# Performance work log

Hardware: AMD Instinct MI355X
Metric: run time of the kernel (lower is better)

Reference implementation:

```python
import jax, jax.numpy as jnp
from jax import lax
import numpy as np


def _pava_pool_idx(y):
    """Pool index per position for the non-decreasing PAVA isotonic fit of 1-D y.
    Stack-based pool-adjacent-violators: sums/cnts hold active pools, top is stack size.
    Returns int pool index (length n) mapping each position to its final pool."""
    n = y.shape[0]

    def step(carry, yi):
        su, ct, top = carry
        su = su.at[top].set(yi)
        ct = ct.at[top].set(1.0)
        top = top + 1

        def cond(s):
            s_, c_, t_ = s
            # violation: mean(pool[t-1]) < mean(pool[t-2]); cross-multiplied (cnts > 0).
            # safe when t_ == 1: index -1 holds zeros -> 0 < 0 is False.
            viol = s_[t_ - 1] * c_[t_ - 2] < s_[t_ - 2] * c_[t_ - 1]
            return (t_ >= 2) & viol

        def body(s):
            s_, c_, t_ = s
            s_ = s_.at[t_ - 2].add(s_[t_ - 1])
            c_ = c_.at[t_ - 2].add(c_[t_ - 1])
            return s_, c_, t_ - 1

        carry = lax.while_loop(cond, body, (su, ct, top))
        return carry, None

    init = (jnp.zeros(n, y.dtype), jnp.zeros(n, y.dtype), jnp.int32(0))
    (su, ct, top), _ = lax.scan(step, init, y)
    # pool j covers positions [ends[j-1], ends[j]); unused pools have ct == 0.
    ends = jnp.cumsum(ct)
    idx = jnp.searchsorted(ends, jnp.arange(n, dtype=ct.dtype), side='right')
    return idx


def _isotonic_nonincreasing_clip0(y):
    """sklearn isotonic_regression(y, y_min=0, increasing=False).
    Pools of the non-increasing fit of y == pools of the non-decreasing fit of -y.
    Final fitted value on each pool is the pool mean of y, clipped at 0."""
    n = y.shape[0]
    idx = _pava_pool_idx(-y)
    sums = jax.ops.segment_sum(y, idx, num_segments=n)
    cnts = jax.ops.segment_sum(jnp.ones_like(y), idx, num_segments=n)
    means = sums / jnp.maximum(cnts, 1.0)
    return jnp.maximum(means[idx], 0.0)


def _prox_owl(beta, weights):
    n = beta.shape[0]
    abs_b = jnp.abs(beta)
    order = jnp.argsort(-abs_b)               # descending |beta|
    iso_in = abs_b[order] - weights
    fit = _isotonic_nonincreasing_clip0(iso_in)
    # inverse permutation: idxs[ix] = arange(n)
    inv = jnp.zeros(n, jnp.int32).at[order].set(jnp.arange(n, dtype=jnp.int32))
    return jnp.sign(beta) * fit[inv]


def reference(u, x, weights):
    diff = (u - x).reshape(-1)
    proxd = _prox_owl(diff, weights)
    return x + proxd.reshape(x.shape)


def setup_inputs() -> dict:
    key = jax.random.key(0)
    k1, k2, k3 = jax.random.split(key, 3)
    shape = (1, 3, 224, 224)
    n = int(np.prod(shape))
    u = jax.random.normal(k1, shape, dtype=jnp.float32)
    x = jax.random.normal(k2, shape, dtype=jnp.float32)
    # OWL weights must be nonincreasing and nonnegative
    w = jnp.sort(jax.random.uniform(k3, (n,), dtype=jnp.float32))[::-1] * 0.01
    return {"u": u, "x": x, "weights": w}
```

## Files before the change

### kernel.cpp

```cpp
#include <hip/hip_runtime.h>
#include <stdint.h>
#include <math.h>

typedef unsigned long long u64;

#define NB 16384
#define BCAP 128
#define NSEG 8192
#define PBLK 64
#define NBLK (NSEG / PBLK)
#define MAXLC 24


__global__ void k_init(const float* __restrict__ u, const float* __restrict__ x,
                       u64* __restrict__ keyPad, int* __restrict__ cursor, int n) {
  int i = blockIdx.x * blockDim.x + threadIdx.x;
  if (i >= n) return;
  float d = u[i] - x[i];
  float ad = fabsf(d);
  u64 key = ((u64)__float_as_uint(ad) << 32) | (unsigned)(~(unsigned)i);
  double v = erf(0.5 * (double)ad);
  int b = (int)(v * (double)NB);
  b = min(max(b, 0), NB - 1);
  int pos = atomicAdd(&cursor[b], 1);
  if (pos < BCAP) keyPad[(size_t)b * BCAP + pos] = key;
}

__global__ void k_scan(const int* __restrict__ cursor, int* __restrict__ descOff) {
  __shared__ int part[1024];
  int t = threadIdx.x;
  const int S = NB / 1024;
  int loc[S];
  int s0 = t * S;
  int sum = 0;
  for (int j = 0; j < S; ++j) { loc[j] = cursor[NB - 1 - (s0 + j)]; sum += loc[j]; }
  part[t] = sum;
  __syncthreads();
  for (int d = 1; d < 1024; d <<= 1) {
    int v = (t >= d) ? part[t - d] : 0;
    __syncthreads();
    part[t] += v;
    __syncthreads();
  }
  int run = part[t] - sum;
  for (int j = 0; j < S; ++j) {
    int b = NB - 1 - (s0 + j);
    descOff[b] = run;
    run += loc[j];
  }
}

__global__ void __launch_bounds__(64) k_bsort(const u64* __restrict__ keyPad,
                                              u64* __restrict__ keyB,
                                              const int* __restrict__ descOff,
                                              const int* __restrict__ cursor) {
  int b = blockIdx.x;
  int cnt = min(cursor[b], BCAP);
  if (cnt == 0) return;
  int start = descOff[b];
  int lane = threadIdx.x;
  const u64* src = keyPad + (size_t)b * BCAP;
  if (cnt == 1) {
    if (lane == 0) keyB[start] = src[0];
    return;
  }
  if (cnt <= 64) {
    int W = 2;
    while (W < cnt) W <<= 1;
    u64 v0 = (lane < cnt) ? src[lane] : 0ull;
    for (int k = 2; k <= W; k <<= 1) {
      for (int j = k >> 1; j >= 1; j >>= 1) {
        bool up = ((lane & j) == 0);
        bool desc = ((lane & k) == 0);
        u64 p = __shfl_xor(v0, j);
        u64 mx = (v0 > p) ? v0 : p, mn = (v0 > p) ? p : v0;
        v0 = (up == desc) ? mx : mn;
      }
    }
    if (lane < cnt) keyB[start + lane] = v0;
  } else {
    u64 v0 = (lane < cnt) ? src[lane] : 0ull;
    u64 v1 = (lane + 64 < cnt) ? src[lane + 64] : 0ull;
    for (int k = 2; k <= 128; k <<= 1) {
      for (int j = k >> 1; j >= 1; j >>= 1) {
        if (j == 64) {
          u64 mx = (v0 > v1) ? v0 : v1;
          u64 mn = (v0 > v1) ? v1 : v0;
          v0 = mx; v1 = mn;
        } else {
          bool up = ((lane & j) == 0);
          bool desc0 = ((lane & k) == 0);
          bool desc1 = (((lane + 64) & k) == 0);
          u64 p0 = __shfl_xor(v0, j);
          u64 p1 = __shfl_xor(v1, j);
          u64 mx0 = (v0 > p0) ? v0 : p0, mn0 = (v0 > p0) ? p0 : v0;
          v0 = (up == desc0) ? mx0 : mn0;
          u64 mx1 = (v1 > p1) ? v1 : p1, mn1 = (v1 > p1) ? p1 : v1;
          v1 = (up == desc1) ? mx1 : mn1;
        }
      }
    }
    if (lane < cnt) keyB[start + lane] = v0;
    if (lane + 64 < cnt) keyB[start + lane + 64] = v1;
  }
}


__device__ __forceinline__ void merge_pair(
    int sL, int sR,
    int* shR, int* stRk, float* shS, float* shC, float* stS, float* stC,
    float* __restrict__ pSum, float* __restrict__ pCnt,
    int* __restrict__ prv, int* __restrict__ nxt) {
  int rR = shR[sR];
  if (rR < 0) return;
  if (shR[sL] < 0) {
    shR[sL] = rR; shS[sL] = shS[sR]; shC[sL] = shC[sR];
    stRk[sL] = stRk[sR]; stS[sL] = stS[sR]; stC[sL] = stC[sR];
    return;
  }
  int lR = stRk[sL];
  float lS = stS[sL], lC = stC[sL];
  float rS = shS[sR], rC = shC[sR];
  nxt[lR] = rR; prv[rR] = lR;
  if (rS * lC > lS * rC) {
    float MS = lS + rS, MC = lC + rC;
    int Mr = lR;
    bool rtail = (rR == stRk[sR]);
    pCnt[rR] = 0.f;
    int nx = nxt[rR];
    nxt[Mr] = nx; if (nx >= 0) prv[nx] = Mr;
    for (;;) {
      int pp = prv[Mr];
      if (pp >= 0) {
        float ps = pSum[pp], pc = pCnt[pp];
        if (MS * pc > ps * MC) {
          MS += ps; MC += pc;
          pCnt[Mr] = 0.f;
          int mn = nxt[Mr];
          nxt[pp] = mn; if (mn >= 0) prv[mn] = pp;
          Mr = pp;
          continue;
        }
      }
      int qq = nxt[Mr];
      if (qq >= 0) {
        float qs = pSum[qq], qc = pCnt[qq];
        if (qs * MC > MS * qc) {
          MS += qs; MC += qc;
          pCnt[qq] = 0.f;
          if (qq == stRk[sR]) rtail = true;
          int qn = nxt[qq];
          nxt[Mr] = qn; if (qn >= 0) prv[qn] = Mr;
          continue;
        }
      }
      break;
    }
    pSum[Mr] = MS; pCnt[Mr] = MC;
    if (Mr == shR[sL]) { shS[sL] = MS; shC[sL] = MC; }
    if (rtail) { stRk[sL] = Mr; stS[sL] = MS; stC[sL] = MC; }
    else       { stRk[sL] = stRk[sR]; stS[sL] = stS[sR]; stC[sL] = stC[sR]; }
  } else {
    stRk[sL] = stRk[sR]; stS[sL] = stS[sR]; stC[sL] = stC[sR];
  }
}

__global__ void __launch_bounds__(64) k_pava_seg(
    const u64* __restrict__ key, const float* __restrict__ w,
    float* __restrict__ pSum, float* __restrict__ pCnt,
    int* __restrict__ prv, int* __restrict__ nxt,
    int* __restrict__ headR2, int* __restrict__ tailR2,
    float* __restrict__ headS2, float* __restrict__ headC2,
    float* __restrict__ tailS2, float* __restrict__ tailC2,
    int n, int Lc, int stride) {
  __shared__ float yv[PBLK * (MAXLC + 1)];
  __shared__ float sS[PBLK * (MAXLC + 1)];
  __shared__ float sC[PBLK * (MAXLC + 1)];
  __shared__ int bHR[PBLK], bTR[PBLK];
  __shared__ float bHS[PBLK], bHC[PBLK], bTS[PBLK], bTC[PBLK];

  int t = threadIdx.x;
  int blk = blockIdx.x;
  int B0 = blk * PBLK * Lc;
  const unsigned* kh = (const unsigned*)key;
  int tot = PBLK * Lc;
  for (int i = t; i < tot; i += PBLK) {
    int g = B0 + i;
    float v = 0.f;
    if (g < n) v = __uint_as_float(kh[2 * g + 1]) - w[g];
    yv[(i / Lc) * stride + (i % Lc)] = v;
  }
  __syncthreads();

  int s = B0 + t * Lc;
  int e = min(s + Lc, n);
  if (s >= e) {
    bHR[t] = -1; bTR[t] = -1;
  } else {
    int cnt = e - s;
    int lb = t * stride;
    float ts = 0.f, tc = 0.f;
    float ss = 0.f, sc = 0.f;
    int depth = 0;
    for (int r = 0; r < cnt; ++r) {
      float v = yv[lb + r];
      if (r > 0) {
        if (depth >= 1) { sS[lb + depth - 1] = ss; sC[lb + depth - 1] = sc; }
        ss = ts; sc = tc; ++depth;
      }
      ts = v; tc = 1.f;
      while (depth >= 1 && ts * sc > ss * tc) {
        ts += ss; tc += sc; --depth;
        if (depth >= 1) { ss = sS[lb + depth - 1]; sc = sC[lb + depth - 1]; }
      }
    }
    int prevStart = -1;
    int start = s;
    float hS = 0.f, hC = 0.f, lS = 0.f, lC = 0.f;
    for (int j = 0; j <= depth; ++j) {
      float sj, cj;
      if (j == depth)          { sj = ts; cj = tc; }
      else if (j == depth - 1) { sj = ss; cj = sc; }
      else                     { sj = sS[lb + j]; cj = sC[lb + j]; }
      if (j == 0) { hS = sj; hC = cj; }
      lS = sj; lC = cj;
      pSum[start] = sj;
      pCnt[start] = cj;
      prv[start] = prevStart;
      if (prevStart >= 0) nxt[prevStart] = start;
      int c = (int)cj;
      for (int z = 1; z < c; ++z) pCnt[start + z] = 0.f;
      prevStart = start;
      start += c;
    }
    nxt[prevStart] = -1;
    bHR[t] = s;  bTR[t] = prevStart;
    bHS[t] = hS; bHC[t] = hC;
    bTS[t] = lS; bTC[t] = lC;
  }
  __syncthreads();
  for (int step = 1; step < PBLK; step <<= 1) {
    int pairs = PBLK / (2 * step);
    if (t < pairs) {
      int sL = t * 2 * step;
      merge_pair(sL, sL + step, bHR, bTR, bHS, bHC, bTS, bTC,
                 pSum, pCnt, prv, nxt);
    }
    __syncthreads();
  }
  if (t == 0) {
    headR2[blk] = bHR[0]; tailR2[blk] = bTR[0];
    headS2[blk] = bHS[0]; headC2[blk] = bHC[0];
    tailS2[blk] = bTS[0]; tailC2[blk] = bTC[0];
  }
}

__global__ void k_merge_pools(float* __restrict__ pSum, float* __restrict__ pCnt,
                              int* __restrict__ prv, int* __restrict__ nxt,
                              const int* __restrict__ headR, const int* __restrict__ tailR,
                              const float* __restrict__ headS, const float* __restrict__ headC,
                              const float* __restrict__ tailS, const float* __restrict__ tailC) {
  __shared__ int shR[NBLK], stRk[NBLK];
  __shared__ float shS[NBLK], shC[NBLK], stS[NBLK], stC[NBLK];
  int t = threadIdx.x;
  if (t < NBLK) {
    shR[t] = headR[t]; stRk[t] = tailR[t];
    shS[t] = headS[t]; shC[t] = headC[t];
    stS[t] = tailS[t]; stC[t] = tailC[t];
  }
  __syncthreads();
  for (int step = 1; step < NBLK; step <<= 1) {
    int pairs = NBLK / (2 * step);
    if (t < pairs) {
      int sL = t * 2 * step;
      merge_pair(sL, sL + step, shR, stRk, shS, shC, stS, stC,
                 pSum, pCnt, prv, nxt);
    }
    __syncthreads();
  }
}

__global__ void k_scatter(const u64* __restrict__ key,
                          const float* __restrict__ pSum, const float* __restrict__ pCnt,
                          const float* __restrict__ u, const float* __restrict__ x,
                          float* __restrict__ out, int n) {
  int i = blockIdx.x * blockDim.x + threadIdx.x;
  if (i >= n) return;
  float c = pCnt[i];
  if (c > 0.f) {
    float m = fmaxf(pSum[i] / c, 0.f);
    int e = i + (int)c;
    for (int k = i; k < e; ++k) {
      unsigned idx = ~(unsigned)(key[k] & 0xFFFFFFFFull);
      float d = u[idx] - x[idx];
      float v = (d > 0.f) ? m : ((d < 0.f) ? -m : 0.f);
      out[idx] = x[idx] + v;
    }
  }
}

extern "C" void kernel_launch(void* const* d_in, const int* in_sizes, int n_in,
                              void* d_out, int out_size, void* d_ws, size_t ws_size,
                              hipStream_t stream) {
  const float* u = (const float*)d_in[0];
  const float* x = (const float*)d_in[1];
  const float* w = (const float*)d_in[2];
  float* out = (float*)d_out;
  int n = in_sizes[0];

  char* base = (char*)d_ws;
  u64* keyPad = (u64*)base;   base += (size_t)NB * BCAP * 8;
  u64* keyB   = (u64*)base;   base += (size_t)n * 8;
  float* pSum = (float*)base; base += (size_t)n * 4;
  float* pCnt = (float*)base; base += (size_t)n * 4;
  int* prv    = (int*)base;   base += (size_t)n * 4;
  int* nxt    = (int*)base;   base += (size_t)n * 4;
  int* cursor = (int*)base;   base += (size_t)NB * 4;
  int* descOff= (int*)base;   base += (size_t)NB * 4;
  int* headR2 = (int*)base;   base += NBLK * 4;
  int* tailR2 = (int*)base;   base += NBLK * 4;
  float* headS2 = (float*)base; base += NBLK * 4;
  float* headC2 = (float*)base; base += NBLK * 4;
  float* tailS2 = (float*)base; base += NBLK * 4;
  float* tailC2 = (float*)base; base += NBLK * 4;

  int gElem = (n + 255) / 256;

  hipMemsetAsync(cursor, 0, NB * sizeof(int), stream);
  hipLaunchKernelGGL(k_init, dim3(gElem), dim3(256), 0, stream,
                     u, x, keyPad, cursor, n);
  hipLaunchKernelGGL(k_scan, dim3(1), dim3(1024), 0, stream,
                     cursor, descOff);
  hipLaunchKernelGGL(k_bsort, dim3(NB), dim3(64), 0, stream,
                     keyPad, keyB, descOff, cursor);

  int Lc = (n + NSEG - 1) / NSEG;
  int stride = (Lc & 1) ? Lc : Lc + 1;
  hipLaunchKernelGGL(k_pava_seg, dim3(NBLK), dim3(PBLK), 0, stream,
                     keyB, w, pSum, pCnt, prv, nxt,
                     headR2, tailR2, headS2, headC2, tailS2, tailC2,
                     n, Lc, stride);
  hipLaunchKernelGGL(k_merge_pools, dim3(1), dim3(NBLK), 0, stream,
                     pSum, pCnt, prv, nxt,
                     headR2, tailR2, headS2, headC2, tailS2, tailC2);
  hipLaunchKernelGGL(k_scatter, dim3(gElem), dim3(256), 0, stream,
                     keyB, pSum, pCnt, u, x, out, n);
}
```

Before: 112.0 us.

## Fold scan and pool-merge into last-block tails, pack sign into sort key

The bucket prefix scan moves into k_init and the cross-block pool merge moves into k_pava_seg. In each case the last block to finish, detected with an atomic counter, does the work, which removes two kernel launches. The bucket count is halved, and the bitonic bucket sort now runs four wavefronts per block. A two-bit sign code is packed into the sort key's index field, so the scatter no longer re-reads u or recomputes the difference. The trade-offs are serial work in a single tail block, reliance on threadfence-based completion detection, and the key index range shrinking to 30 bits.

Measured after the change: 181.9 us. +62.4%, slower.

```diff
diff --git a/kernel.cpp b/kernel.cpp
--- a/kernel.cpp
+++ b/kernel.cpp
@@ -4,107 +4,12 @@
 
 typedef unsigned long long u64;
 
-#define NB 16384
+#define NB 8192
 #define BCAP 128
 #define NSEG 8192
 #define PBLK 64
 #define NBLK (NSEG / PBLK)
 #define MAXLC 24
-
-
-__global__ void k_init(const float* __restrict__ u, const float* __restrict__ x,
-                       u64* __restrict__ keyPad, int* __restrict__ cursor, int n) {
-  int i = blockIdx.x * blockDim.x + threadIdx.x;
-  if (i >= n) return;
-  float d = u[i] - x[i];
-  float ad = fabsf(d);
-  u64 key = ((u64)__float_as_uint(ad) << 32) | (unsigned)(~(unsigned)i);
-  double v = erf(0.5 * (double)ad);
-  int b = (int)(v * (double)NB);
-  b = min(max(b, 0), NB - 1);
-  int pos = atomicAdd(&cursor[b], 1);
-  if (pos < BCAP) keyPad[(size_t)b * BCAP + pos] = key;
-}
-
-__global__ void k_scan(const int* __restrict__ cursor, int* __restrict__ descOff) {
-  __shared__ int part[1024];
-  int t = threadIdx.x;
-  const int S = NB / 1024;
-  int loc[S];
-  int s0 = t * S;
-  int sum = 0;
-  for (int j = 0; j < S; ++j) { loc[j] = cursor[NB - 1 - (s0 + j)]; sum += loc[j]; }
-  part[t] = sum;
-  __syncthreads();
-  for (int d = 1; d < 1024; d <<= 1) {
-    int v = (t >= d) ? part[t - d] : 0;
-    __syncthreads();
-    part[t] += v;
-    __syncthreads();
-  }
-  int run = part[t] - sum;
-  for (int j = 0; j < S; ++j) {
-    int b = NB - 1 - (s0 + j);
-    descOff[b] = run;
-    run += loc[j];
-  }
-}
-
-__global__ void __launch_bounds__(64) k_bsort(const u64* __restrict__ keyPad,
-                                              u64* __restrict__ keyB,
-                                              const int* __restrict__ descOff,
-                                              const int* __restrict__ cursor) {
-  int b = blockIdx.x;
-  int cnt = min(cursor[b], BCAP);
-  if (cnt == 0) return;
-  int start = descOff[b];
-  int lane = threadIdx.x;
-  const u64* src = keyPad + (size_t)b * BCAP;
-  if (cnt == 1) {
-    if (lane == 0) keyB[start] = src[0];
-    return;
-  }
-  if (cnt <= 64) {
-    int W = 2;
-    while (W < cnt) W <<= 1;
-    u64 v0 = (lane < cnt) ? src[lane] : 0ull;
-    for (int k = 2; k <= W; k <<= 1) {
-      for (int j = k >> 1; j >= 1; j >>= 1) {
-        bool up = ((lane & j) == 0);
-        bool desc = ((lane & k) == 0);
-        u64 p = __shfl_xor(v0, j);
-        u64 mx = (v0 > p) ? v0 : p, mn = (v0 > p) ? p : v0;
-        v0 = (up == desc) ? mx : mn;
-      }
-    }
-    if (lane < cnt) keyB[start + lane] = v0;
-  } else {
-    u64 v0 = (lane < cnt) ? src[lane] : 0ull;
-    u64 v1 = (lane + 64 < cnt) ? src[lane + 64] : 0ull;
-    for (int k = 2; k <= 128; k <<= 1) {
-      for (int j = k >> 1; j >= 1; j >>= 1) {
-        if (j == 64) {
-          u64 mx = (v0 > v1) ? v0 : v1;
-          u64 mn = (v0 > v1) ? v1 : v0;
-          v0 = mx; v1 = mn;
-        } else {
-          bool up = ((lane & j) == 0);
-          bool desc0 = ((lane & k) == 0);
-          bool desc1 = (((lane + 64) & k) == 0);
-          u64 p0 = __shfl_xor(v0, j);
-          u64 p1 = __shfl_xor(v1, j);
-          u64 mx0 = (v0 > p0) ? v0 : p0, mn0 = (v0 > p0) ? p0 : v0;
-          v0 = (up == desc0) ? mx0 : mn0;
-          u64 mx1 = (v1 > p1) ? v1 : p1, mn1 = (v1 > p1) ? p1 : v1;
-          v1 = (up == desc1) ? mx1 : mn1;
-        }
-      }
-    }
-    if (lane < cnt) keyB[start + lane] = v0;
-    if (lane + 64 < cnt) keyB[start + lane + 64] = v1;
-  }
-}
-
 
 __device__ __forceinline__ void merge_pair(
     int sL, int sR,
@@ -165,6 +70,116 @@
   }
 }
 
+__device__ __forceinline__ void wave_bsort(const u64* src, u64* dst,
+                                           int start, int cnt, int lane) {
+  if (cnt == 1) {
+    if (lane == 0) dst[start] = src[0];
+    return;
+  }
+  if (cnt <= 64) {
+    int W = 2;
+    while (W < cnt) W <<= 1;
+    u64 v0 = (lane < cnt) ? src[lane] : 0ull;
+    for (int k = 2; k <= W; k <<= 1) {
+      for (int j = k >> 1; j >= 1; j >>= 1) {
+        bool up = ((lane & j) == 0);
+        bool desc = ((lane & k) == 0);
+        u64 p = __shfl_xor(v0, j);
+        u64 mx = (v0 > p) ? v0 : p, mn = (v0 > p) ? p : v0;
+        v0 = (up == desc) ? mx : mn;
+      }
+    }
+    if (lane < cnt) dst[start + lane] = v0;
+  } else {
+    u64 v0 = (lane < cnt) ? src[lane] : 0ull;
+    u64 v1 = (lane + 64 < cnt) ? src[lane + 64] : 0ull;
+    for (int k = 2; k <= 128; k <<= 1) {
+      for (int j = k >> 1; j >= 1; j >>= 1) {
+        if (j == 64) {
+          u64 mx = (v0 > v1) ? v0 : v1;
+          u64 mn = (v0 > v1) ? v1 : v0;
+          v0 = mx; v1 = mn;
+        } else {
+          bool up = ((lane & j) == 0);
+          bool desc0 = ((lane & k) == 0);
+          bool desc1 = (((lane + 64) & k) == 0);
+          u64 p0 = __shfl_xor(v0, j);
+          u64 p1 = __shfl_xor(v1, j);
+          u64 mx0 = (v0 > p0) ? v0 : p0, mn0 = (v0 > p0) ? p0 : v0;
+          v0 = (up == desc0) ? mx0 : mn0;
+          u64 mx1 = (v1 > p1) ? v1 : p1, mn1 = (v1 > p1) ? p1 : v1;
+          v1 = (up == desc1) ? mx1 : mn1;
+        }
+      }
+    }
+    if (lane < cnt) dst[start + lane] = v0;
+    if (lane + 64 < cnt) dst[start + lane + 64] = v1;
+  }
+}
+
+__global__ void k_init(const float* __restrict__ u, const float* __restrict__ x,
+                       u64* __restrict__ keyPad, int* __restrict__ cursor,
+                       int* __restrict__ done, int* __restrict__ descOff, int n) {
+  int i = blockIdx.x * blockDim.x + threadIdx.x;
+  int t = threadIdx.x;
+  if (i < n) {
+    float d = u[i] - x[i];
+    float ad = fabsf(d);
+    unsigned code = (d > 0.f) ? 2u : ((d < 0.f) ? 0u : 1u);
+    u64 key = ((u64)__float_as_uint(ad) << 32) |
+              (unsigned)(~(((unsigned)i << 2) | code));
+    double v = erf(0.5 * (double)ad);
+    int b = (int)(v * (double)NB);
+    b = min(max(b, 0), NB - 1);
+    int pos = atomicAdd(&cursor[b], 1);
+    if (pos < BCAP) keyPad[(size_t)b * BCAP + pos] = key;
+  }
+  __shared__ int isLast;
+  __shared__ int part[256];
+  __syncthreads();
+  __threadfence();
+  if (t == 0) {
+    int old = atomicAdd(done, 1);
+    isLast = (old == (int)gridDim.x - 1) ? 1 : 0;
+  }
+  __syncthreads();
+  if (!isLast) return;
+  __threadfence();
+  const int S = NB / 256;
+  int loc[S];
+  int s0 = t * S;
+  int sum = 0;
+  for (int j = 0; j < S; ++j) {
+    loc[j] = cursor[NB - 1 - (s0 + j)];
+    sum += loc[j];
+  }
+  part[t] = sum;
+  __syncthreads();
+  for (int d = 1; d < 256; d <<= 1) {
+    int v = (t >= d) ? part[t - d] : 0;
+    __syncthreads();
+    part[t] += v;
+    __syncthreads();
+  }
+  int run = part[t] - sum;
+  for (int j = 0; j < S; ++j) {
+    int b = NB - 1 - (s0 + j);
+    descOff[b] = run;
+    run += loc[j];
+  }
+}
+
+__global__ void __launch_bounds__(256) k_bsort(const u64* __restrict__ keyPad,
+                                               u64* __restrict__ keyB,
+                                               const int* __restrict__ descOff,
+                                               const int* __restrict__ cursor) {
+  int wv = threadIdx.x >> 6, lane = threadIdx.x & 63;
+  int b = blockIdx.x * 4 + wv;
+  int cnt = min(cursor[b], BCAP);
+  if (cnt == 0) return;
+  wave_bsort(keyPad + (size_t)b * BCAP, keyB, descOff[b], cnt, lane);
+}
+
 __global__ void __launch_bounds__(64) k_pava_seg(
     const u64* __restrict__ key, const float* __restrict__ w,
     float* __restrict__ pSum, float* __restrict__ pCnt,
@@ -172,12 +187,13 @@
     int* __restrict__ headR2, int* __restrict__ tailR2,
     float* __restrict__ headS2, float* __restrict__ headC2,
     float* __restrict__ tailS2, float* __restrict__ tailC2,
-    int n, int Lc, int stride) {
-  __shared__ float yv[PBLK * (MAXLC + 1)];
-  __shared__ float sS[PBLK * (MAXLC + 1)];
-  __shared__ float sC[PBLK * (MAXLC + 1)];
+    int* __restrict__ done, int n, int Lc, int stride) {
+  __shared__ float yv[PBLK * MAXLC], sS[PBLK * MAXLC], sC[PBLK * MAXLC];
   __shared__ int bHR[PBLK], bTR[PBLK];
   __shared__ float bHS[PBLK], bHC[PBLK], bTS[PBLK], bTC[PBLK];
+  __shared__ int mR[NBLK], mT[NBLK];
+  __shared__ float mHS[NBLK], mHC[NBLK], mTS[NBLK], mTC[NBLK];
+  __shared__ int isLast;
 
   int t = threadIdx.x;
   int blk = blockIdx.x;
@@ -191,7 +207,6 @@
     yv[(i / Lc) * stride + (i % Lc)] = v;
   }
   __syncthreads();
-
   int s = B0 + t * Lc;
   int e = min(s + Lc, n);
   if (s >= e) {
@@ -199,8 +214,7 @@
   } else {
     int cnt = e - s;
     int lb = t * stride;
-    float ts = 0.f, tc = 0.f;
-    float ss = 0.f, sc = 0.f;
+    float ts = 0.f, tc = 0.f, ss = 0.f, sc = 0.f;
     int depth = 0;
     for (int r = 0; r < cnt; ++r) {
       float v = yv[lb + r];
@@ -224,8 +238,7 @@
       else                     { sj = sS[lb + j]; cj = sC[lb + j]; }
       if (j == 0) { hS = sj; hC = cj; }
       lS = sj; lC = cj;
-      pSum[start] = sj;
-      pCnt[start] = cj;
+      pSum[start] = sj; pCnt[start] = cj;
       prv[start] = prevStart;
       if (prevStart >= 0) nxt[prevStart] = start;
       int c = (int)cj;
@@ -243,8 +256,7 @@
     int pairs = PBLK / (2 * step);
     if (t < pairs) {
       int sL = t * 2 * step;
-      merge_pair(sL, sL + step, bHR, bTR, bHS, bHC, bTS, bTC,
-                 pSum, pCnt, prv, nxt);
+      merge_pair(sL, sL + step, bHR, bTR, bHS, bHC, bTS, bTC, pSum, pCnt, prv, nxt);
     }
     __syncthreads();
   }
@@ -253,28 +265,26 @@
     headS2[blk] = bHS[0]; headC2[blk] = bHC[0];
     tailS2[blk] = bTS[0]; tailC2[blk] = bTC[0];
   }
-}
-
-__global__ void k_merge_pools(float* __restrict__ pSum, float* __restrict__ pCnt,
-                              int* __restrict__ prv, int* __restrict__ nxt,
-                              const int* __restrict__ headR, const int* __restrict__ tailR,
-                              const float* __restrict__ headS, const float* __restrict__ headC,
-                              const float* __restrict__ tailS, const float* __restrict__ tailC) {
-  __shared__ int shR[NBLK], stRk[NBLK];
-  __shared__ float shS[NBLK], shC[NBLK], stS[NBLK], stC[NBLK];
-  int t = threadIdx.x;
-  if (t < NBLK) {
-    shR[t] = headR[t]; stRk[t] = tailR[t];
-    shS[t] = headS[t]; shC[t] = headC[t];
-    stS[t] = tailS[t]; stC[t] = tailC[t];
+  __syncthreads();
+  __threadfence();
+  if (t == 0) {
+    int old = atomicAdd(done, 1);
+    isLast = (old == NBLK - 1) ? 1 : 0;
+  }
+  __syncthreads();
+  if (!isLast) return;
+  __threadfence();
+  for (int i = t; i < NBLK; i += PBLK) {
+    mR[i] = headR2[i]; mT[i] = tailR2[i];
+    mHS[i] = headS2[i]; mHC[i] = headC2[i];
+    mTS[i] = tailS2[i]; mTC[i] = tailC2[i];
   }
   __syncthreads();
   for (int step = 1; step < NBLK; step <<= 1) {
     int pairs = NBLK / (2 * step);
-    if (t < pairs) {
-      int sL = t * 2 * step;
-      merge_pair(sL, sL + step, shR, stRk, shS, shC, stS, stC,
-                 pSum, pCnt, prv, nxt);
+    for (int p = t; p < pairs; p += PBLK) {
+      int sL = p * 2 * step;
+      merge_pair(sL, sL + step, mR, mT, mHS, mHC, mTS, mTC, pSum, pCnt, prv, nxt);
     }
     __syncthreads();
   }
@@ -282,8 +292,7 @@
 
 __global__ void k_scatter(const u64* __restrict__ key,
                           const float* __restrict__ pSum, const float* __restrict__ pCnt,
-                          const float* __restrict__ u, const float* __restrict__ x,
-                          float* __restrict__ out, int n) {
+                          const float* __restrict__ x, float* __restrict__ out, int n) {
   int i = blockIdx.x * blockDim.x + threadIdx.x;
   if (i >= n) return;
   float c = pCnt[i];
@@ -291,9 +300,10 @@
     float m = fmaxf(pSum[i] / c, 0.f);
     int e = i + (int)c;
     for (int k = i; k < e; ++k) {
-      unsigned idx = ~(unsigned)(key[k] & 0xFFFFFFFFull);
-      float d = u[idx] - x[idx];
-      float v = (d > 0.f) ? m : ((d < 0.f) ? -m : 0.f);
+      unsigned r = ~(unsigned)(key[k] & 0xFFFFFFFFull);
+      unsigned idx = r >> 2;
+      unsigned code = r & 3u;
+      float v = (code == 2u) ? m : ((code == 0u) ? -m : 0.f);
       out[idx] = x[idx] + v;
     }
   }
@@ -315,7 +325,7 @@
   float* pCnt = (float*)base; base += (size_t)n * 4;
   int* prv    = (int*)base;   base += (size_t)n * 4;
   int* nxt    = (int*)base;   base += (size_t)n * 4;
-  int* cursor = (int*)base;   base += (size_t)NB * 4;
+  int* cursor = (int*)base;   base += (size_t)(NB + 2) * 4;
   int* descOff= (int*)base;   base += (size_t)NB * 4;
   int* headR2 = (int*)base;   base += NBLK * 4;
   int* tailR2 = (int*)base;   base += NBLK * 4;
@@ -323,26 +333,22 @@
   float* headC2 = (float*)base; base += NBLK * 4;
   float* tailS2 = (float*)base; base += NBLK * 4;
   float* tailC2 = (float*)base; base += NBLK * 4;
+  int* done1 = cursor + NB;
+  int* done2 = cursor + NB + 1;
 
   int gElem = (n + 255) / 256;
-
-  hipMemsetAsync(cursor, 0, NB * sizeof(int), stream);
-  hipLaunchKernelGGL(k_init, dim3(gElem), dim3(256), 0, stream,
-                     u, x, keyPad, cursor, n);
-  hipLaunchKernelGGL(k_scan, dim3(1), dim3(1024), 0, stream,
-                     cursor, descOff);
-  hipLaunchKernelGGL(k_bsort, dim3(NB), dim3(64), 0, stream,
-                     keyPad, keyB, descOff, cursor);
-
   int Lc = (n + NSEG - 1) / NSEG;
   int stride = (Lc & 1) ? Lc : Lc + 1;
+
+  hipMemsetAsync(cursor, 0, (size_t)(NB + 2) * 4, stream);
+  hipLaunchKernelGGL(k_init, dim3(gElem), dim3(256), 0, stream,
+                     u, x, keyPad, cursor, done1, descOff, n);
+  hipLaunchKernelGGL(k_bsort, dim3(NB / 4), dim3(256), 0, stream,
+                     keyPad, keyB, descOff, cursor);
   hipLaunchKernelGGL(k_pava_seg, dim3(NBLK), dim3(PBLK), 0, stream,
                      keyB, w, pSum, pCnt, prv, nxt,
                      headR2, tailR2, headS2, headC2, tailS2, tailC2,
-                     n, Lc, stride);
-  hipLaunchKernelGGL(k_merge_pools, dim3(1), dim3(NBLK), 0, stream,
-                     pSum, pCnt, prv, nxt,
-                     headR2, tailR2, headS2, headC2, tailS2, tailC2);
+                     done2, n, Lc, stride);
   hipLaunchKernelGGL(k_scatter, dim3(gElem), dim3(256), 0, stream,
-                     keyB, pSum, pCnt, u, x, out, n);
-}
+                     keyB, pSum, pCnt, x, out, n);
+}
```
